# Performance work log

Hardware: AMD Instinct MI355X
Metric: run time of the kernel (lower is better)

Reference implementation:

```python
import jax, jax.numpy as jnp
import numpy as np

DIM = 2048
NH = 16
NKV = 4
HD = DIM // NH  # 128
ROPE_BASE = 10000.0
QK_GAIN_INIT = 1.0


def setup_inputs() -> dict:
    key = jax.random.key(0)
    ks = jax.random.split(key, 6)
    kv_dim = NKV * HD
    s = 0.02
    return {
        "x": jax.random.normal(ks[0], (2, 2048, DIM), dtype=jnp.float32),
        "wq": jax.random.normal(ks[1], (DIM, DIM), dtype=jnp.float32) * s,
        "wk": jax.random.normal(ks[2], (kv_dim, DIM), dtype=jnp.float32) * s,
        "wv": jax.random.normal(ks[3], (kv_dim, DIM), dtype=jnp.float32) * s,
        "wproj": jax.random.normal(ks[4], (DIM, DIM), dtype=jnp.float32) * s,
        "q_gain": jnp.full((NH,), QK_GAIN_INIT, dtype=jnp.float32),
    }


def _rms_norm(t):
    eps = jnp.asarray(jnp.finfo(t.dtype).eps, t.dtype)
    ms = jnp.mean(jnp.square(t), axis=-1, keepdims=True)
    return t * jax.lax.rsqrt(ms + eps)


def _rope_tables(seqlen, dtype):
    inv_freq = 1.0 / (ROPE_BASE ** (np.arange(0, HD, 2, dtype=np.float32) / HD))
    t = np.arange(seqlen, dtype=np.float32)
    freqs = np.outer(t, inv_freq)  # [S, HD/2]
    cos = jnp.asarray(np.cos(freqs), dtype=dtype)[None, None]  # [1,1,S,HD/2]
    sin = jnp.asarray(np.sin(freqs), dtype=dtype)[None, None]
    return cos, sin


def _apply_rotary(x, cos, sin):
    half = x.shape[-1] // 2
    x1, x2 = x[..., :half], x[..., half:]
    return jnp.concatenate((x1 * cos + x2 * sin, -x1 * sin + x2 * cos), axis=-1)


def reference(x, wq, wk, wv, wproj, q_gain):
    B, S, D = x.shape
    # projections (torch F.linear: x @ W.T), reshape to [B, H, S, HD]
    q = (x @ wq.T).reshape(B, S, NH, HD).transpose(0, 2, 1, 3)
    k = (x @ wk.T).reshape(B, S, NKV, HD).transpose(0, 2, 1, 3)
    v = (x @ wv.T).reshape(B, S, NKV, HD).transpose(0, 2, 1, 3)
    q = _rms_norm(q)
    k = _rms_norm(k)
    cos, sin = _rope_tables(S, q.dtype)
    q = _apply_rotary(q, cos, sin)
    k = _apply_rotary(k, cos, sin)
    q = q * q_gain.astype(q.dtype)[None, :, None, None]
    # GQA: expand kv heads
    G = NH // NKV
    k = jnp.repeat(k, G, axis=1)  # [B, NH, S, HD]
    v = jnp.repeat(v, G, axis=1)
    scale = 1.0 / np.sqrt(HD)
    scores = jnp.einsum("bhsd,bhtd->bhst", q, k) * scale
    causal = jnp.tril(jnp.ones((S, S), dtype=bool))
    scores = jnp.where(causal[None, None], scores, jnp.finfo(scores.dtype).min)
    attn = jax.nn.softmax(scores, axis=-1)
    y = jnp.einsum("bhst,bhtd->bhsd", attn, v)
    y = y.transpose(0, 2, 1, 3).reshape(B, S, D)
    return y @ wproj.T
```

## Files before the change

### kernel.cpp

```cpp
#include <hip/hip_runtime.h>
#include <hip/hip_bf16.h>
#include <stdint.h>

#define DIM 2048
#define NH 16
#define NKV 4
#define HD 128
#define BATCH 2
#define SEQ 2048

typedef unsigned short ushort_t;
typedef __attribute__((ext_vector_type(8))) short short8;
typedef __attribute__((ext_vector_type(4))) float f32x4;
typedef __attribute__((ext_vector_type(16))) float f32x16;

__device__ inline ushort_t f2b(float f) {
    union { float f; uint32_t u; } v; v.f = f;
    uint32_t r = (v.u + 0x7fffu + ((v.u >> 16) & 1u)) >> 16;
    return (ushort_t)r;
}

__device__ inline float fexp2(float x) {
#if __has_builtin(__builtin_amdgcn_exp2f)
    return __builtin_amdgcn_exp2f(x);
#else
    float r; asm("v_exp_f32 %0, %1" : "=v"(r) : "v"(x)); return r;
#endif
}

__global__ void cast_all(const float* __restrict__ x, const float* __restrict__ wq,
                         const float* __restrict__ wk, const float* __restrict__ wv,
                         const float* __restrict__ wp,
                         ushort_t* __restrict__ xb, ushort_t* __restrict__ wqkvb,
                         ushort_t* __restrict__ wprojb) {
    const int stride = gridDim.x * blockDim.x;
    for (int i = blockIdx.x * blockDim.x + threadIdx.x; i < 4718592; i += stride) {
        const float* s; ushort_t* d; int off;
        if (i < 2097152)      { s = x;  d = xb;               off = i; }
        else if (i < 3145728) { s = wq; d = wqkvb;            off = i - 2097152; }
        else if (i < 3407872) { s = wk; d = wqkvb + 4194304;  off = i - 3145728; }
        else if (i < 3670016) { s = wv; d = wqkvb + 5242880;  off = i - 3407872; }
        else                  { s = wp; d = wprojb;           off = i - 3670016; }
        float4 v = ((const float4*)s)[off];
        ushort4 o;
        o.x = f2b(v.x); o.y = f2b(v.y); o.z = f2b(v.z); o.w = f2b(v.w);
        ((ushort4*)d)[off] = o;
    }
}

__device__ inline void gload_lds16(const ushort_t* g, ushort_t* l) {
    __builtin_amdgcn_global_load_lds((const __attribute__((address_space(1))) void*)g,
                                     (__attribute__((address_space(3))) void*)l, 16, 0, 0);
}

__launch_bounds__(256, 2)
__global__ void gemm_bt(const ushort_t* __restrict__ A, const ushort_t* __restrict__ Bm,
                        float* __restrict__ C, int M, int N, int K) {
    __shared__ ushort_t lA[128 * 32];
    __shared__ ushort_t lB[128 * 32];
    const int t = threadIdx.x;
    const int lane = t & 63;
    const int w = t >> 6;
    const int wr = w >> 1, wc = w & 1;
    const int g = lane >> 4, l16 = lane & 15;
    const int nwg = gridDim.x * gridDim.y;
    const int bid = blockIdx.y * gridDim.x + blockIdx.x;
    const int cpx = nwg >> 3;
    const int swz = (bid & 7) * cpx + (bid >> 3);
    const int nbx = gridDim.x;
    const int m0 = (swz / nbx) * 128, n0 = (swz % nbx) * 128;

    f32x4 acc[4][4];
#pragma unroll
    for (int i = 0; i < 4; i++)
#pragma unroll
        for (int j = 0; j < 4; j++) acc[i][j] = (f32x4){0, 0, 0, 0};

    const int row_a = t >> 2;
    const int col_a = (t & 3) * 8;
    const int nk = K >> 5;

    for (int kt = 0; kt < nk; ++kt) {
        const int k0 = kt * 32;
        gload_lds16(A + (size_t)(m0 + row_a) * K + k0 + col_a,       lA + t * 8);
        gload_lds16(A + (size_t)(m0 + 64 + row_a) * K + k0 + col_a,  lA + 2048 + t * 8);
        gload_lds16(Bm + (size_t)(n0 + row_a) * K + k0 + col_a,      lB + t * 8);
        gload_lds16(Bm + (size_t)(n0 + 64 + row_a) * K + k0 + col_a, lB + 2048 + t * 8);
        __syncthreads();
        short8 af[4], bf[4];
#pragma unroll
        for (int i = 0; i < 4; i++) {
            af[i] = *(const short8*)(lA + (wr * 64 + i * 16 + l16) * 32 + g * 8);
            bf[i] = *(const short8*)(lB + (wc * 64 + i * 16 + l16) * 32 + g * 8);
        }
#pragma unroll
        for (int i = 0; i < 4; i++)
#pragma unroll
            for (int j = 0; j < 4; j++)
                acc[i][j] = __builtin_amdgcn_mfma_f32_16x16x32_bf16(af[i], bf[j], acc[i][j], 0, 0, 0);
        __syncthreads();
    }
#pragma unroll
    for (int i = 0; i < 4; i++)
#pragma unroll
        for (int j = 0; j < 4; j++) {
            int rb = m0 + wr * 64 + i * 16 + g * 4;
            int cb = n0 + wc * 64 + j * 16 + l16;
#pragma unroll
            for (int r = 0; r < 4; r++)
                C[(size_t)(rb + r) * N + cb] = acc[i][j][r];
        }
}

__launch_bounds__(256, 2)
__global__ void gemm_qkv(const ushort_t* __restrict__ A, const ushort_t* __restrict__ Bm,
                         const float* __restrict__ qgain,
                         ushort_t* __restrict__ qb, ushort_t* __restrict__ kb,
                         ushort_t* __restrict__ vtb) {
    const int K = 2048;
    __shared__ ushort_t lA[128 * 32];
    __shared__ ushort_t lB[128 * 32];
    __shared__ float psum[2][128];
    const int t = threadIdx.x;
    const int lane = t & 63;
    const int w = t >> 6;
    const int wr = w >> 1, wc = w & 1;
    const int g = lane >> 4, l16 = lane & 15;
    const int nwg = gridDim.x * gridDim.y;
    const int bid = blockIdx.y * gridDim.x + blockIdx.x;
    const int cpx = nwg >> 3;
    const int swz = (bid & 7) * cpx + (bid >> 3);
    const int nt = swz % 24;
    const int m0 = (swz / 24) * 128, n0 = nt * 128;

    int cm[4];
    cm[0] = wc * 32 + l16;
    cm[1] = wc * 32 + 16 + l16;
    cm[2] = cm[0] + 64;
    cm[3] = cm[1] + 64;

    f32x4 acc[4][4];
#pragma unroll
    for (int i = 0; i < 4; i++)
#pragma unroll
        for (int j = 0; j < 4; j++) acc[i][j] = (f32x4){0, 0, 0, 0};

    const int row_a = t >> 2;
    const int col_a = (t & 3) * 8;

    for (int kt = 0; kt < (K >> 5); ++kt) {
        const int k0 = kt * 32;
        gload_lds16(A + (size_t)(m0 + row_a) * K + k0 + col_a,       lA + t * 8);
        gload_lds16(A + (size_t)(m0 + 64 + row_a) * K + k0 + col_a,  lA + 2048 + t * 8);
        gload_lds16(Bm + (size_t)(n0 + row_a) * K + k0 + col_a,      lB + t * 8);
        gload_lds16(Bm + (size_t)(n0 + 64 + row_a) * K + k0 + col_a, lB + 2048 + t * 8);
        __syncthreads();
        short8 af[4], bf[4];
#pragma unroll
        for (int i = 0; i < 4; i++) {
            af[i] = *(const short8*)(lA + (wr * 64 + i * 16 + l16) * 32 + g * 8);
            bf[i] = *(const short8*)(lB + cm[i] * 32 + g * 8);
        }
#pragma unroll
        for (int i = 0; i < 4; i++)
#pragma unroll
            for (int j = 0; j < 4; j++)
                acc[i][j] = __builtin_amdgcn_mfma_f32_16x16x32_bf16(af[i], bf[j], acc[i][j], 0, 0, 0);
        __syncthreads();
    }

    const int b = m0 >> 11;
    const int s0 = m0 & 2047;

    if (nt < 20) {
        float ssq[4][4];
#pragma unroll
        for (int i = 0; i < 4; i++)
#pragma unroll
            for (int r = 0; r < 4; r++) {
                float v = 0.0f;
#pragma unroll
                for (int j = 0; j < 4; j++) v += acc[i][j][r] * acc[i][j][r];
#pragma unroll
                for (int m = 1; m < 16; m <<= 1) v += __shfl_xor(v, m, 64);
                ssq[i][r] = v;
            }
        if (l16 == 0) {
#pragma unroll
            for (int i = 0; i < 4; i++)
#pragma unroll
                for (int r = 0; r < 4; r++)
                    psum[wc][wr * 64 + i * 16 + g * 4 + r] = ssq[i][r];
        }
        __syncthreads();

        const float gsc = (nt < 16) ? qgain[nt] * (0.08838834764831845f * 1.4426950408889634f)
                                    : 1.0f;
        ushort_t* outp = (nt < 16) ? qb + (size_t)(b * NH + nt) * SEQ * HD
                                   : kb + (size_t)(b * NKV + (nt - 16)) * SEQ * HD;
        const float inv0 = exp2f(-(float)cm[0] * (13.287712379549449f / 64.0f));
        const float inv1 = exp2f(-(float)cm[1] * (13.287712379549449f / 64.0f));
#pragma unroll
        for (int i = 0; i < 4; i++)
#pragma unroll
            for (int r = 0; r < 4; r++) {
                const int sloc = wr * 64 + i * 16 + g * 4 + r;
                const float tot = psum[0][sloc] + psum[1][sloc];
                const float rg = rsqrtf(tot * (1.0f / 128.0f) + 1.1920929e-07f) * gsc;
                const float fs = (float)(s0 + sloc);
                ushort_t* orow = outp + (size_t)(s0 + sloc) * HD;
#pragma unroll
                for (int jp = 0; jp < 2; jp++) {
                    float x1 = acc[i][jp][r], x2 = acc[i][jp + 2][r];
                    float sn, c;
                    __sincosf(fs * (jp ? inv1 : inv0), &sn, &c);
                    orow[cm[jp]]      = f2b((x1 * c + x2 * sn) * rg);
                    orow[cm[jp] + 64] = f2b((x2 * c - x1 * sn) * rg);
                }
            }
    } else {
        ushort_t* vout = vtb + (size_t)((b * NKV + (nt - 20)) * HD) * SEQ;
#pragma unroll
        for (int i = 0; i < 4; i++)
#pragma unroll
            for (int j = 0; j < 4; j++) {
                ushort4 o;
                o.x = f2b(acc[i][j][0]); o.y = f2b(acc[i][j][1]);
                o.z = f2b(acc[i][j][2]); o.w = f2b(acc[i][j][3]);
                *(ushort4*)(vout + (size_t)cm[j] * SEQ + s0 + wr * 64 + i * 16 + g * 4) = o;
            }
    }
}

#define KVB 64

__launch_bounds__(256, 2)
__global__ void attn(const ushort_t* __restrict__ qbuf, const ushort_t* __restrict__ kbuf,
                     const ushort_t* __restrict__ vtbuf, ushort_t* __restrict__ ybuf) {
    __shared__ ushort_t Klds[KVB * HD];
    __shared__ ushort_t Vlds[HD * KVB];

    const int idx = blockIdx.x;
    const int pass = idx >> 8;
    const int rr0 = idx & 255;
    const int xcd = rr0 & 7;
    const int jj = rr0 >> 5;
    const int qt = pass ? jj : 15 - jj;
    const int bh = xcd * 4 + ((rr0 >> 3) & 3);
    const int b = bh >> 4, hh = bh & 15;
    const int kvh = hh >> 2;
    const int t = threadIdx.x;
    const int w = t >> 6, lane = t & 63;
    const int l31 = lane & 31, hf = lane >> 5;
    const int q0 = qt * 128;
    const int qbase = q0 + w * 32;

    const ushort_t* Qp = qbuf + (size_t)(b * NH + hh) * SEQ * HD;
    const ushort_t* Kp = kbuf + (size_t)(b * NKV + kvh) * SEQ * HD;
    const ushort_t* Vtp = vtbuf + (size_t)(b * NKV + kvh) * HD * SEQ;

    short8 aq[8];
#pragma unroll
    for (int dc = 0; dc < 8; dc++)
        aq[dc] = *(const short8*)(Qp + (size_t)(qbase + l31) * HD + dc * 16 + hf * 8);

    f32x16 y[4];
#pragma unroll
    for (int db = 0; db < 4; db++)
#pragma unroll
        for (int r = 0; r < 16; r++) y[db][r] = 0.0f;
    float mrun = -1e30f, lrun = 0.0f;

    const int krow = t >> 4;
    const int kcol = ((t & 15) ^ (t >> 4)) * 8;
    const int vrow = t >> 3;
    const int vcol = ((t & 7) ^ ((t >> 3) & 7)) * 8;

    const int ntiles = q0 / 64 + 2;
    for (int kt = 0; kt < ntiles; ++kt) {
        const int kv0 = kt * KVB;
        __syncthreads();
#pragma unroll
        for (int i = 0; i < 4; i++) {
            gload_lds16(Kp + (size_t)(kv0 + i * 16 + krow) * HD + kcol, Klds + i * 2048 + t * 8);
            gload_lds16(Vtp + (size_t)(i * 32 + vrow) * SEQ + kv0 + vcol, Vlds + i * 2048 + t * 8);
        }
        __syncthreads();
        if (kv0 > qbase + 31) continue;

        f32x16 s0v, s1v;
#pragma unroll
        for (int r = 0; r < 16; r++) { s0v[r] = 0.0f; s1v[r] = 0.0f; }
#pragma unroll
        for (int dc = 0; dc < 8; dc++) {
            short8 ak0 = *(const short8*)(Klds + (size_t)(l31) * HD      + (((dc * 2 + hf) ^ (l31 & 15)) * 8));
            short8 ak1 = *(const short8*)(Klds + (size_t)(32 + l31) * HD + (((dc * 2 + hf) ^ (l31 & 15)) * 8));
            s0v = __builtin_amdgcn_mfma_f32_32x32x16_bf16(ak0, aq[dc], s0v, 0, 0, 0);
            s1v = __builtin_amdgcn_mfma_f32_32x32x16_bf16(ak1, aq[dc], s1v, 0, 0, 0);
        }

        const int qabs = qbase + l31;
        if (kv0 + 63 > qbase) {
#pragma unroll
            for (int r = 0; r < 16; r++) {
                int kvr = kv0 + (r & 3) + 8 * (r >> 2) + 4 * hf;
                if (kvr > qabs)      s0v[r] = -1e30f;
                if (kvr + 32 > qabs) s1v[r] = -1e30f;
            }
        }

        float mt = -1e30f;
#pragma unroll
        for (int r = 0; r < 16; r++) mt = fmaxf(mt, fmaxf(s0v[r], s1v[r]));
        mt = fmaxf(mt, __shfl_xor(mt, 32, 64));
        if (!__all(mt <= mrun + 8.0f)) {
            float mn = fmaxf(mrun, mt);
            float al = fexp2(mrun - mn);
            mrun = mn;
            lrun *= al;
#pragma unroll
            for (int r = 0; r < 16; r++) {
                float alr = __shfl(al, (r & 3) + 8 * (r >> 2) + 4 * hf, 64);
#pragma unroll
                for (int db = 0; db < 4; db++) y[db][r] *= alr;
            }
        }
        float sum = 0.0f;
#pragma unroll
        for (int r = 0; r < 16; r++) {
            float p0 = fexp2(s0v[r] - mrun);
            float p1 = fexp2(s1v[r] - mrun);
            s0v[r] = p0; s1v[r] = p1;
            sum += p0 + p1;
        }
        sum += __shfl_xor(sum, 32, 64);
        lrun += sum;

        union PW { short8 v; uint32_t wd[4]; } pa[4];
#pragma unroll
        for (int blk = 0; blk < 2; blk++) {
#pragma unroll
            for (int ks2 = 0; ks2 < 2; ks2++) {
#pragma unroll
                for (int t2 = 0; t2 < 2; t2++) {
                    float a0 = blk ? s1v[8 * ks2 + 2 * t2]         : s0v[8 * ks2 + 2 * t2];
                    float a1 = blk ? s1v[8 * ks2 + 2 * t2 + 1]     : s0v[8 * ks2 + 2 * t2 + 1];
                    float b0 = blk ? s1v[8 * ks2 + 4 + 2 * t2]     : s0v[8 * ks2 + 4 + 2 * t2];
                    float b1 = blk ? s1v[8 * ks2 + 4 + 2 * t2 + 1] : s0v[8 * ks2 + 4 + 2 * t2 + 1];
                    uint32_t pw = (uint32_t)f2b(a0) | ((uint32_t)f2b(a1) << 16);
                    uint32_t qw = (uint32_t)f2b(b0) | ((uint32_t)f2b(b1) << 16);
                    uint32_t send = hf ? pw : qw;
                    uint32_t recv = (uint32_t)__shfl_xor((int)send, 32, 64);
                    pa[blk * 2 + ks2].wd[t2]     = hf ? recv : pw;
                    pa[blk * 2 + ks2].wd[t2 + 2] = hf ? qw : recv;
                }
            }
        }

#pragma unroll
        for (int ks = 0; ks < 4; ks++) {
#pragma unroll
            for (int db = 0; db < 4; db++) {
                short8 bv = *(const short8*)(Vlds + (size_t)(db * 32 + l31) * KVB
                                             + (((ks * 2 + hf) ^ (l31 & 7)) * 8));
                y[db] = __builtin_amdgcn_mfma_f32_32x32x16_bf16(pa[ks].v, bv, y[db], 0, 0, 0);
            }
        }
    }

    float linv = 1.0f / lrun;
    ushort_t* Yp = ybuf + (size_t)b * SEQ * DIM + hh * HD;
#pragma unroll
    for (int r = 0; r < 16; r++) {
        int qloc = (r & 3) + 8 * (r >> 2) + 4 * hf;
        float lr = __shfl(linv, qloc, 64);
        int q = qbase + qloc;
#pragma unroll
        for (int db = 0; db < 4; db++)
            Yp[(size_t)q * DIM + db * 32 + l31] = f2b(y[db][r] * lr);
    }
}

extern "C" void kernel_launch(void* const* d_in, const int* in_sizes, int n_in,
                              void* d_out, int out_size, void* d_ws, size_t ws_size,
                              hipStream_t stream) {
    (void)in_sizes; (void)n_in; (void)out_size; (void)ws_size;
    const float* x     = (const float*)d_in[0];
    const float* wq    = (const float*)d_in[1];
    const float* wk    = (const float*)d_in[2];
    const float* wv    = (const float*)d_in[3];
    const float* wproj = (const float*)d_in[4];
    const float* qg    = (const float*)d_in[5];

    char* ws = (char*)d_ws;
    ushort_t* xb     = (ushort_t*)ws;
    ushort_t* wqkvb  = (ushort_t*)(ws + (16u << 20));
    ushort_t* wprojb = (ushort_t*)(ws + (28u << 20));
    ushort_t* qb     = (ushort_t*)(ws + (36u << 20));
    ushort_t* kb     = (ushort_t*)(ws + (52u << 20));
    ushort_t* vtb    = (ushort_t*)(ws + (56u << 20));
    ushort_t* yb     = (ushort_t*)(ws + (60u << 20));

    cast_all<<<2048, 256, 0, stream>>>(x, wq, wk, wv, wproj, xb, wqkvb, wprojb);
    gemm_qkv<<<dim3(24, 32), 256, 0, stream>>>(xb, wqkvb, qg, qb, kb, vtb);
    attn<<<512, 256, 0, stream>>>(qb, kb, vtb, yb);
    gemm_bt<<<dim3(16, 32), 256, 0, stream>>>(yb, wprojb, (float*)d_out, 4096, 2048, 2048);
}
```

Baseline: 198.0 us.

## Deepen GEMM K-tiles with swizzled LDS and register-prefetch attention K/V tiles

Both projection GEMMs now stage 64-wide K slices instead of 32, with an XOR swizzle on the LDS column chunk. This halves the number of barrier pairs per K loop and is meant to avoid LDS bank conflicts on the fragment reads. The attention kernel drops direct global-to-LDS loads for K and V. It now prefetches the next tile into registers while computing the current one, then writes those registers to swizzled LDS after the barrier, so global latency overlaps with MFMA work. The cost is higher LDS use in the GEMMs and more live registers in attention, which may reduce occupancy.

New measurement: 174.4 us. 1.14x faster.

```diff
diff --git a/kernel.cpp b/kernel.cpp
--- a/kernel.cpp
+++ b/kernel.cpp
@@ -56,8 +56,8 @@
 __launch_bounds__(256, 2)
 __global__ void gemm_bt(const ushort_t* __restrict__ A, const ushort_t* __restrict__ Bm,
                         float* __restrict__ C, int M, int N, int K) {
-    __shared__ ushort_t lA[128 * 32];
-    __shared__ ushort_t lB[128 * 32];
+    __shared__ ushort_t lA[128 * 64];
+    __shared__ ushort_t lB[128 * 64];
     const int t = threadIdx.x;
     const int lane = t & 63;
     const int w = t >> 6;
@@ -76,29 +76,34 @@
 #pragma unroll
         for (int j = 0; j < 4; j++) acc[i][j] = (f32x4){0, 0, 0, 0};
 
-    const int row_a = t >> 2;
-    const int col_a = (t & 3) * 8;
-    const int nk = K >> 5;
-
-    for (int kt = 0; kt < nk; ++kt) {
-        const int k0 = kt * 32;
-        gload_lds16(A + (size_t)(m0 + row_a) * K + k0 + col_a,       lA + t * 8);
-        gload_lds16(A + (size_t)(m0 + 64 + row_a) * K + k0 + col_a,  lA + 2048 + t * 8);
-        gload_lds16(Bm + (size_t)(n0 + row_a) * K + k0 + col_a,      lB + t * 8);
-        gload_lds16(Bm + (size_t)(n0 + 64 + row_a) * K + k0 + col_a, lB + 2048 + t * 8);
-        __syncthreads();
-        short8 af[4], bf[4];
+    const int row_s = t >> 3;
+    const int cx = t & 7;
+    const int xr = (lane & 7);
+
+    for (int kt = 0; kt < (K >> 6); ++kt) {
+        const int k0 = kt * 64;
+        __syncthreads();
 #pragma unroll
         for (int i = 0; i < 4; i++) {
-            af[i] = *(const short8*)(lA + (wr * 64 + i * 16 + l16) * 32 + g * 8);
-            bf[i] = *(const short8*)(lB + (wc * 64 + i * 16 + l16) * 32 + g * 8);
-        }
-#pragma unroll
-        for (int i = 0; i < 4; i++)
-#pragma unroll
-            for (int j = 0; j < 4; j++)
-                acc[i][j] = __builtin_amdgcn_mfma_f32_16x16x32_bf16(af[i], bf[j], acc[i][j], 0, 0, 0);
-        __syncthreads();
+            const int ra = i * 32 + row_s;
+            gload_lds16(A + (size_t)(m0 + ra) * K + k0 + ((cx ^ (row_s & 7)) * 8), lA + i * 2048 + t * 8);
+            gload_lds16(Bm + (size_t)(n0 + ra) * K + k0 + ((cx ^ (row_s & 7)) * 8), lB + i * 2048 + t * 8);
+        }
+        __syncthreads();
+#pragma unroll
+        for (int kk = 0; kk < 2; kk++) {
+            short8 af[4], bf[4];
+#pragma unroll
+            for (int i = 0; i < 4; i++) {
+                af[i] = *(const short8*)(lA + (wr * 64 + i * 16 + l16) * 64 + (((kk * 4 + g) ^ xr) * 8));
+                bf[i] = *(const short8*)(lB + (wc * 64 + i * 16 + l16) * 64 + (((kk * 4 + g) ^ xr) * 8));
+            }
+#pragma unroll
+            for (int i = 0; i < 4; i++)
+#pragma unroll
+                for (int j = 0; j < 4; j++)
+                    acc[i][j] = __builtin_amdgcn_mfma_f32_16x16x32_bf16(af[i], bf[j], acc[i][j], 0, 0, 0);
+        }
     }
 #pragma unroll
     for (int i = 0; i < 4; i++)
@@ -118,8 +123,8 @@
                          ushort_t* __restrict__ qb, ushort_t* __restrict__ kb,
                          ushort_t* __restrict__ vtb) {
     const int K = 2048;
-    __shared__ ushort_t lA[128 * 32];
-    __shared__ ushort_t lB[128 * 32];
+    __shared__ ushort_t lA[128 * 64];
+    __shared__ ushort_t lB[128 * 64];
     __shared__ float psum[2][128];
     const int t = threadIdx.x;
     const int lane = t & 63;
@@ -145,28 +150,34 @@
 #pragma unroll
         for (int j = 0; j < 4; j++) acc[i][j] = (f32x4){0, 0, 0, 0};
 
-    const int row_a = t >> 2;
-    const int col_a = (t & 3) * 8;
-
-    for (int kt = 0; kt < (K >> 5); ++kt) {
-        const int k0 = kt * 32;
-        gload_lds16(A + (size_t)(m0 + row_a) * K + k0 + col_a,       lA + t * 8);
-        gload_lds16(A + (size_t)(m0 + 64 + row_a) * K + k0 + col_a,  lA + 2048 + t * 8);
-        gload_lds16(Bm + (size_t)(n0 + row_a) * K + k0 + col_a,      lB + t * 8);
-        gload_lds16(Bm + (size_t)(n0 + 64 + row_a) * K + k0 + col_a, lB + 2048 + t * 8);
-        __syncthreads();
-        short8 af[4], bf[4];
+    const int row_s = t >> 3;
+    const int cx = t & 7;
+    const int xr = (lane & 7);
+
+    for (int kt = 0; kt < (K >> 6); ++kt) {
+        const int k0 = kt * 64;
+        __syncthreads();
 #pragma unroll
         for (int i = 0; i < 4; i++) {
-            af[i] = *(const short8*)(lA + (wr * 64 + i * 16 + l16) * 32 + g * 8);
-            bf[i] = *(const short8*)(lB + cm[i] * 32 + g * 8);
-        }
-#pragma unroll
-        for (int i = 0; i < 4; i++)
-#pragma unroll
-            for (int j = 0; j < 4; j++)
-                acc[i][j] = __builtin_amdgcn_mfma_f32_16x16x32_bf16(af[i], bf[j], acc[i][j], 0, 0, 0);
-        __syncthreads();
+            const int ra = i * 32 + row_s;
+            gload_lds16(A + (size_t)(m0 + ra) * K + k0 + ((cx ^ (row_s & 7)) * 8), lA + i * 2048 + t * 8);
+            gload_lds16(Bm + (size_t)(n0 + ra) * K + k0 + ((cx ^ (row_s & 7)) * 8), lB + i * 2048 + t * 8);
+        }
+        __syncthreads();
+#pragma unroll
+        for (int kk = 0; kk < 2; kk++) {
+            short8 af[4], bf[4];
+#pragma unroll
+            for (int i = 0; i < 4; i++) {
+                af[i] = *(const short8*)(lA + (wr * 64 + i * 16 + l16) * 64 + (((kk * 4 + g) ^ xr) * 8));
+                bf[i] = *(const short8*)(lB + cm[i] * 64 + (((kk * 4 + g) ^ xr) * 8));
+            }
+#pragma unroll
+            for (int i = 0; i < 4; i++)
+#pragma unroll
+                for (int j = 0; j < 4; j++)
+                    acc[i][j] = __builtin_amdgcn_mfma_f32_16x16x32_bf16(af[i], bf[j], acc[i][j], 0, 0, 0);
+        }
     }
 
     const int b = m0 >> 11;
@@ -271,99 +282,121 @@
         for (int r = 0; r < 16; r++) y[db][r] = 0.0f;
     float mrun = -1e30f, lrun = 0.0f;
 
-    const int krow = t >> 4;
-    const int kcol = ((t & 15) ^ (t >> 4)) * 8;
-    const int vrow = t >> 3;
-    const int vcol = ((t & 7) ^ ((t >> 3) & 7)) * 8;
-
+    const int k_row = t >> 2;
+    const int k_c0 = (t & 3) * 4;
+    const int v_row = t >> 1;
+    const int v_c0 = (t & 1) * 4;
+
+    short8 kreg[4], vreg[4];
     const int ntiles = q0 / 64 + 2;
+
+#pragma unroll
+    for (int i = 0; i < 4; i++) {
+        kreg[i] = *(const short8*)(Kp + (size_t)k_row * HD + (k_c0 + i) * 8);
+        vreg[i] = *(const short8*)(Vtp + (size_t)v_row * SEQ + (v_c0 + i) * 8);
+    }
+
     for (int kt = 0; kt < ntiles; ++kt) {
         const int kv0 = kt * KVB;
         __syncthreads();
-#pragma unroll
-        for (int i = 0; i < 4; i++) {
-            gload_lds16(Kp + (size_t)(kv0 + i * 16 + krow) * HD + kcol, Klds + i * 2048 + t * 8);
-            gload_lds16(Vtp + (size_t)(i * 32 + vrow) * SEQ + kv0 + vcol, Vlds + i * 2048 + t * 8);
-        }
-        __syncthreads();
-        if (kv0 > qbase + 31) continue;
-
-        f32x16 s0v, s1v;
-#pragma unroll
-        for (int r = 0; r < 16; r++) { s0v[r] = 0.0f; s1v[r] = 0.0f; }
-#pragma unroll
-        for (int dc = 0; dc < 8; dc++) {
-            short8 ak0 = *(const short8*)(Klds + (size_t)(l31) * HD      + (((dc * 2 + hf) ^ (l31 & 15)) * 8));
-            short8 ak1 = *(const short8*)(Klds + (size_t)(32 + l31) * HD + (((dc * 2 + hf) ^ (l31 & 15)) * 8));
-            s0v = __builtin_amdgcn_mfma_f32_32x32x16_bf16(ak0, aq[dc], s0v, 0, 0, 0);
-            s1v = __builtin_amdgcn_mfma_f32_32x32x16_bf16(ak1, aq[dc], s1v, 0, 0, 0);
-        }
-
-        const int qabs = qbase + l31;
-        if (kv0 + 63 > qbase) {
+        {
+            ushort_t* kd = Klds + k_row * HD;
+            ushort_t* vd = Vlds + v_row * KVB;
+#pragma unroll
+            for (int i = 0; i < 4; i++)
+                *(short8*)(kd + (((k_c0 + i) ^ (k_row & 15)) * 8)) = kreg[i];
+#pragma unroll
+            for (int i = 0; i < 4; i++)
+                *(short8*)(vd + (((v_c0 + i) ^ (v_row & 7)) * 8)) = vreg[i];
+        }
+        __syncthreads();
+        if (kt + 1 < ntiles) {
+            const int nkv0 = kv0 + KVB;
+#pragma unroll
+            for (int i = 0; i < 4; i++) {
+                kreg[i] = *(const short8*)(Kp + (size_t)(nkv0 + k_row) * HD + (k_c0 + i) * 8);
+                vreg[i] = *(const short8*)(Vtp + (size_t)v_row * SEQ + nkv0 + (v_c0 + i) * 8);
+            }
+        }
+
+        if (kv0 <= qbase + 31) {
+            f32x16 s0v, s1v;
+#pragma unroll
+            for (int r = 0; r < 16; r++) { s0v[r] = 0.0f; s1v[r] = 0.0f; }
+#pragma unroll
+            for (int dc = 0; dc < 8; dc++) {
+                short8 ak0 = *(const short8*)(Klds + (size_t)(l31) * HD      + (((dc * 2 + hf) ^ (l31 & 15)) * 8));
+                short8 ak1 = *(const short8*)(Klds + (size_t)(32 + l31) * HD + (((dc * 2 + hf) ^ (l31 & 15)) * 8));
+                s0v = __builtin_amdgcn_mfma_f32_32x32x16_bf16(ak0, aq[dc], s0v, 0, 0, 0);
+                s1v = __builtin_amdgcn_mfma_f32_32x32x16_bf16(ak1, aq[dc], s1v, 0, 0, 0);
+            }
+
+            const int qabs = qbase + l31;
+            if (kv0 + 63 > qbase) {
+#pragma unroll
+                for (int r = 0; r < 16; r++) {
+                    int kvr = kv0 + (r & 3) + 8 * (r >> 2) + 4 * hf;
+                    if (kvr > qabs)      s0v[r] = -1e30f;
+                    if (kvr + 32 > qabs) s1v[r] = -1e30f;
+                }
+            }
+
+            float mt = -1e30f;
+#pragma unroll
+            for (int r = 0; r < 16; r++) mt = fmaxf(mt, fmaxf(s0v[r], s1v[r]));
+            mt = fmaxf(mt, __shfl_xor(mt, 32, 64));
+            if (!__all(mt <= mrun + 8.0f)) {
+                float mn = fmaxf(mrun, mt);
+                float al = fexp2(mrun - mn);
+                mrun = mn;
+                lrun *= al;
+#pragma unroll
+                for (int r = 0; r < 16; r++) {
+                    float alr = __shfl(al, (r & 3) + 8 * (r >> 2) + 4 * hf, 64);
+#pragma unroll
+                    for (int db = 0; db < 4; db++) y[db][r] *= alr;
+                }
+            }
+            float sum = 0.0f;
 #pragma unroll
             for (int r = 0; r < 16; r++) {
-                int kvr = kv0 + (r & 3) + 8 * (r >> 2) + 4 * hf;
-                if (kvr > qabs)      s0v[r] = -1e30f;
-                if (kvr + 32 > qabs) s1v[r] = -1e30f;
-            }
-        }
-
-        float mt = -1e30f;
-#pragma unroll
-        for (int r = 0; r < 16; r++) mt = fmaxf(mt, fmaxf(s0v[r], s1v[r]));
-        mt = fmaxf(mt, __shfl_xor(mt, 32, 64));
-        if (!__all(mt <= mrun + 8.0f)) {
-            float mn = fmaxf(mrun, mt);
-            float al = fexp2(mrun - mn);
-            mrun = mn;
-            lrun *= al;
-#pragma unroll
-            for (int r = 0; r < 16; r++) {
-                float alr = __shfl(al, (r & 3) + 8 * (r >> 2) + 4 * hf, 64);
-#pragma unroll
-                for (int db = 0; db < 4; db++) y[db][r] *= alr;
-            }
-        }
-        float sum = 0.0f;
-#pragma unroll
-        for (int r = 0; r < 16; r++) {
-            float p0 = fexp2(s0v[r] - mrun);
-            float p1 = fexp2(s1v[r] - mrun);
-            s0v[r] = p0; s1v[r] = p1;
-            sum += p0 + p1;
-        }
-        sum += __shfl_xor(sum, 32, 64);
-        lrun += sum;
-
-        union PW { short8 v; uint32_t wd[4]; } pa[4];
-#pragma unroll
-        for (int blk = 0; blk < 2; blk++) {
-#pragma unroll
-            for (int ks2 = 0; ks2 < 2; ks2++) {
-#pragma unroll
-                for (int t2 = 0; t2 < 2; t2++) {
-                    float a0 = blk ? s1v[8 * ks2 + 2 * t2]         : s0v[8 * ks2 + 2 * t2];
-                    float a1 = blk ? s1v[8 * ks2 + 2 * t2 + 1]     : s0v[8 * ks2 + 2 * t2 + 1];
-                    float b0 = blk ? s1v[8 * ks2 + 4 + 2 * t2]     : s0v[8 * ks2 + 4 + 2 * t2];
-                    float b1 = blk ? s1v[8 * ks2 + 4 + 2 * t2 + 1] : s0v[8 * ks2 + 4 + 2 * t2 + 1];
-                    uint32_t pw = (uint32_t)f2b(a0) | ((uint32_t)f2b(a1) << 16);
-                    uint32_t qw = (uint32_t)f2b(b0) | ((uint32_t)f2b(b1) << 16);
-                    uint32_t send = hf ? pw : qw;
-                    uint32_t recv = (uint32_t)__shfl_xor((int)send, 32, 64);
-                    pa[blk * 2 + ks2].wd[t2]     = hf ? recv : pw;
-                    pa[blk * 2 + ks2].wd[t2 + 2] = hf ? qw : recv;
+                float p0 = fexp2(s0v[r] - mrun);
+                float p1 = fexp2(s1v[r] - mrun);
+                s0v[r] = p0; s1v[r] = p1;
+                sum += p0 + p1;
+            }
+            sum += __shfl_xor(sum, 32, 64);
+            lrun += sum;
+
+            union PW { short8 v; uint32_t wd[4]; } pa[4];
+#pragma unroll
+            for (int blk = 0; blk < 2; blk++) {
+#pragma unroll
+                for (int ks2 = 0; ks2 < 2; ks2++) {
+#pragma unroll
+                    for (int t2 = 0; t2 < 2; t2++) {
+                        float a0 = blk ? s1v[8 * ks2 + 2 * t2]         : s0v[8 * ks2 + 2 * t2];
+                        float a1 = blk ? s1v[8 * ks2 + 2 * t2 + 1]     : s0v[8 * ks2 + 2 * t2 + 1];
+                        float b0 = blk ? s1v[8 * ks2 + 4 + 2 * t2]     : s0v[8 * ks2 + 4 + 2 * t2];
+                        float b1 = blk ? s1v[8 * ks2 + 4 + 2 * t2 + 1] : s0v[8 * ks2 + 4 + 2 * t2 + 1];
+                        uint32_t pw = (uint32_t)f2b(a0) | ((uint32_t)f2b(a1) << 16);
+                        uint32_t qw = (uint32_t)f2b(b0) | ((uint32_t)f2b(b1) << 16);
+                        uint32_t send = hf ? pw : qw;
+                        uint32_t recv = (uint32_t)__shfl_xor((int)send, 32, 64);
+                        pa[blk * 2 + ks2].wd[t2]     = hf ? recv : pw;
+                        pa[blk * 2 + ks2].wd[t2 + 2] = hf ? qw : recv;
+                    }
                 }
             }
-        }
-
-#pragma unroll
-        for (int ks = 0; ks < 4; ks++) {
-#pragma unroll
-            for (int db = 0; db < 4; db++) {
-                short8 bv = *(const short8*)(Vlds + (size_t)(db * 32 + l31) * KVB
-                                             + (((ks * 2 + hf) ^ (l31 & 7)) * 8));
-                y[db] = __builtin_amdgcn_mfma_f32_32x32x16_bf16(pa[ks].v, bv, y[db], 0, 0, 0);
+
+#pragma unroll
+            for (int ks = 0; ks < 4; ks++) {
+#pragma unroll
+                for (int db = 0; db < 4; db++) {
+                    short8 bv = *(const short8*)(Vlds + (size_t)(db * 32 + l31) * KVB
+                                                 + (((ks * 2 + hf) ^ (l31 & 7)) * 8));
+                    y[db] = __builtin_amdgcn_mfma_f32_32x32x16_bf16(pa[ks].v, bv, y[db], 0, 0, 0);
+                }
             }
         }
     }
```
